# Kernel tuning notes

Measured on AMD Instinct MI355X. Metric: run time of the kernel, lower is better.

Reference implementation:

```python
import jax, jax.numpy as jnp
import numpy as np

B, N, NC = 8, 25200, 80           # YOLOv5-640 / COCO raw output
CONF_THRES = 0.25                  # init conf_threshold
IOU_THRES = 0.45                   # init iou_threshold
PATCH_CONF = 0.001                 # hard-coded patch_conf in forward
GN = jnp.array([640.0, 640.0, 640.0, 640.0], dtype=jnp.float32)  # img_size[[1,0,1,0]]
MAX_WH = 4096.0                    # class offset for class-aware NMS
K_CLEAN = 512                      # fixed-size cap on NMS candidates (clean branch)
K_PATCH = 1024                     # fixed-size cap on NMS candidates (patch branch)
MAX_DET_CLEAN = 1000
MAX_DET_PATCH = 30000
NEG = jnp.float32(-1e30)


def _xywh2xyxy(x):
    xy, wh = x[..., :2], x[..., 2:4]
    return jnp.concatenate([xy - wh * 0.5, xy + wh * 0.5], axis=-1)


def _pairwise_iou(a, b):
    # a: [A,4] xyxy, b: [B,4] xyxy -> [A,B] jaccard overlap
    tl = jnp.maximum(a[:, None, :2], b[None, :, :2])
    br = jnp.minimum(a[:, None, 2:4], b[None, :, 2:4])
    wh = jnp.clip(br - tl, 0.0)
    inter = wh[..., 0] * wh[..., 1]
    area_a = (a[:, 2] - a[:, 0]) * (a[:, 3] - a[:, 1])
    area_b = (b[:, 2] - b[:, 0]) * (b[:, 3] - b[:, 1])
    union = area_a[:, None] + area_b[None, :] - inter
    union = jnp.where(union > 0, union, 1.0)  # guard degenerate boxes
    return inter / union


def _nms_single(pred, conf_thres, K, max_det):
    # pred: [N, 5+nc]. Fixed-size (padded/masked) greedy NMS, class-aware via MAX_WH offset.
    obj = pred[:, 4]
    cls_conf = pred[:, 5:] * obj[:, None]          # x[:,5:] *= x[:,4:5]
    conf = jnp.max(cls_conf, axis=-1)
    cls = jnp.argmax(cls_conf, axis=-1)
    box = _xywh2xyxy(pred[:, :4])
    valid = (obj > conf_thres) & (conf > conf_thres)
    scores = jnp.where(valid, conf, NEG)
    top_scores, idx = jax.lax.top_k(scores, K)     # sorted desc, like torchvision NMS ordering
    boxes = box[idx]
    cls_k = cls[idx]
    valid_k = top_scores > conf_thres
    boxes_off = boxes + cls_k.astype(boxes.dtype)[:, None] * MAX_WH
    iou = jax.lax.stop_gradient(_pairwise_iou(boxes_off, boxes_off))
    ar = jnp.arange(K)

    def step(keep, i):
        sup = keep[i] & (iou[i] > IOU_THRES) & (ar > i)
        return keep & (~sup), None

    keep, _ = jax.lax.scan(step, valid_k, jnp.arange(K))
    rank = jnp.cumsum(keep.astype(jnp.int32))
    keep = keep & (rank <= max_det)
    return boxes, cls_k, keep


def _image_loss(cb, cc, ck, pb, pc, pk):
    # per clean detection: max IoU over kept patch boxes of the same class (0 if none)
    iou = _pairwise_iou(cb / GN, pb / GN)          # [K_CLEAN, K_PATCH]
    mask = ck[:, None] & pk[None, :] & (cc[:, None] == pc[None, :])
    tm = jnp.max(jnp.where(mask, iou, 0.0), axis=1)
    s = jnp.sum(jnp.where(ck, tm, 0.0))
    n = jnp.sum(ck.astype(jnp.float32))
    return s, n


def _forward(output_clean, output_patch):
    cb, cc, ck = jax.vmap(lambda p: _nms_single(p, CONF_THRES, K_CLEAN, MAX_DET_CLEAN))(output_clean)
    pb, pc, pk = jax.vmap(lambda p: _nms_single(p, PATCH_CONF, K_PATCH, MAX_DET_PATCH))(output_patch)
    s, n = jax.vmap(_image_loss)(cb, cc, ck, pb, pc, pk)
    total, cnt = jnp.sum(s), jnp.sum(n)
    return jnp.where(cnt > 0, 1.0 - total / jnp.maximum(cnt, 1.0), jnp.float32(1.0))


def _make_pred(key):
    ka, kb, kc, kd = jax.random.split(key, 4)
    cxcy = jax.random.uniform(ka, (B, N, 2), jnp.float32, 20.0, 620.0)
    wh = jax.random.uniform(kb, (B, N, 2), jnp.float32, 2.0, 150.0)
    obj = jax.random.uniform(kc, (B, N, 1), jnp.float32)
    clsp = jax.random.uniform(kd, (B, N, NC), jnp.float32)
    return jnp.concatenate([cxcy, wh, obj, clsp], axis=-1)


def setup_inputs() -> dict:
    key = jax.random.key(0)
    k1, k2 = jax.random.split(key)
    return {"output_clean": _make_pred(k1), "output_patch": _make_pred(k2)}


def reference(output_clean, output_patch):
    return _forward(output_clean, output_patch)
```

## Files before the change

kernel.cpp:

```cpp
#include <hip/hip_runtime.h>


static constexpr int NB   = 8;
static constexpr int NA   = 25200;
static constexpr int NCLS = 80;
static constexpr int CH   = 85;
static constexpr int NT   = 16;
static constexpr int KMAX = 1024;
static constexpr int NBIN = 32768;
static constexpr int PSH  = 17;
static constexpr int CAP  = 2048;
static constexpr int IOB  = 34;

static constexpr size_t OFF_KEYS = 0;
static constexpr size_t OFF_CLS  = OFF_KEYS + (size_t)NT * NA * 4;
static constexpr size_t OFF_BOX  = OFF_CLS  + (size_t)NT * NA * 4;
static constexpr size_t OFF_CLSK = OFF_BOX  + (size_t)NT * KMAX * 16;
static constexpr size_t OFF_VALK = OFF_CLSK + (size_t)NT * KMAX * 4;
static constexpr size_t OFF_KEEP = OFF_VALK + (size_t)NT * KMAX * 4;
static constexpr size_t OFF_SUP  = OFF_KEEP + (size_t)NT * 16 * 8;
static constexpr size_t OFF_DIAG = OFF_SUP  + (size_t)NT * KMAX * 16 * 8;
static constexpr size_t OFF_PART = OFF_DIAG + (size_t)NT * KMAX * 8;
static constexpr size_t OFF_CNT  = OFF_PART + 512;

__device__ __forceinline__ unsigned okey(float f) {
  unsigned u = __float_as_uint(f);
  return (u & 0x80000000u) ? ~u : (u | 0x80000000u);
}

__device__ __forceinline__ unsigned long long shflx64(unsigned long long v, int m) {
  unsigned lo = (unsigned)v, hi = (unsigned)(v >> 32);
  lo = __shfl_xor(lo, m);
  hi = __shfl_xor(hi, m);
  return ((unsigned long long)hi << 32) | lo;
}

__global__ __launch_bounds__(256) void k_score(const float* __restrict__ clean,
                                               const float* __restrict__ patch,
                                               unsigned* __restrict__ keys,
                                               int* __restrict__ clsArr,
                                               unsigned* __restrict__ cnt) {
#pragma clang fp contract(off)
  if (blockIdx.x == 0 && blockIdx.y == 0 && threadIdx.x == 0) *cnt = 0u;
  __shared__ float rows[4][32 * CH];
  const int t    = blockIdx.y;
  const int wave = threadIdx.x >> 6;
  const int lane = threadIdx.x & 63;
  const int a0   = blockIdx.x * 128 + wave * 32;
  if (a0 >= NA) return;
  const int nA = (NA - a0 < 32) ? (NA - a0) : 32;
  const float conf_th = (t < 8) ? 0.25f : 0.001f;
  const float* __restrict__ src = ((t < 8) ? clean : patch) + (size_t)(t & 7) * NA * CH;
  const float4* g4 = (const float4*)(src + (size_t)a0 * CH);
  float4* rows4 = (float4*)rows[wave];
  const int n4 = (nA * CH) >> 2;
#pragma unroll
  for (int c = 0; c < 11; ++c) {
    const int i = (c << 6) + lane;
    if (i < n4) {
      __builtin_amdgcn_global_load_lds(
          (const __attribute__((address_space(1))) void*)(g4 + i),
          (__attribute__((address_space(3))) void*)(rows4 + (c << 6)),
          16, 0, 2 );
    }
  }
  asm volatile("s_waitcnt vmcnt(0)" ::: "memory");
  __builtin_amdgcn_sched_barrier(0);

  const int ar = lane >> 1;
  const int q  = lane & 1;
  if (ar < nA) {
    const float* r = rows[wave] + ar * CH;
    const float obj = r[4];
    const int c0 = q * 40;
    float best = r[5 + c0] * obj;
    int bc = c0;
    for (int c = c0 + 1; c < c0 + 40; ++c) {
      float v = r[5 + c] * obj;
      if (v > best) { best = v; bc = c; }
    }
    float b1 = __shfl_down(best, 1); int c1 = __shfl_down(bc, 1);
    if (b1 > best || (b1 == best && c1 < bc)) { best = b1; bc = c1; }
    if (q == 0) {
      const bool valid = (obj > conf_th) && (best > conf_th);
      const float score = valid ? best : -1e30f;
      const int a = a0 + ar;
      keys[(size_t)t * NA + a]   = okey(score);
      clsArr[(size_t)t * NA + a] = bc;
    }
  }
}

__global__ __launch_bounds__(1024) void k_topsel(const unsigned* __restrict__ keys,
                                                 const int* __restrict__ clsArr,
                                                 const float* __restrict__ clean,
                                                 const float* __restrict__ patch,
                                                 float* __restrict__ boxesK,
                                                 int* __restrict__ clsK,
                                                 int* __restrict__ validK) {
#pragma clang fp contract(off)
  const int t = blockIdx.x;
  const unsigned K = (t < 8) ? 512u : 1024u;
  const float conf_th = (t < 8) ? 0.25f : 0.001f;
  __shared__ unsigned h32[NBIN / 2];
  __shared__ unsigned long long buf[CAP];
  __shared__ unsigned scnt[2];
  __shared__ unsigned wtot[16], wsuf[16];
  __shared__ int s_chunk;
  __shared__ unsigned s_acc, s_B;
  const int tid = threadIdx.x;
  const int lane = tid & 63, wv = tid >> 6;
  for (int i = tid; i < NBIN / 2; i += 1024) h32[i] = 0u;
  for (int i = tid; i < CAP; i += 1024) buf[i] = 0ull;
  if (tid < 2) scnt[tid] = 0u;
  __syncthreads();
  const unsigned INVKEY = okey(-1e30f);
  const unsigned* kv = keys + (size_t)t * NA;
  {
    const uint4* kv4 = (const uint4*)kv;
    unsigned invCnt = 0;
    for (int i = tid; i < NA / 4; i += 1024) {
      uint4 kq = kv4[i];
      unsigned kk[4] = {kq.x, kq.y, kq.z, kq.w};
#pragma unroll
      for (int c = 0; c < 4; ++c) {
        if (kk[c] == INVKEY) {
          ++invCnt;
        } else {
          unsigned b = kk[c] >> PSH;
          atomicAdd(&h32[b >> 1], 1u << ((b & 1) * 16));
        }
      }
    }
    for (int off = 32; off > 0; off >>= 1) invCnt += __shfl_down(invCnt, off);
    if (lane == 0 && invCnt) {
      unsigned b = INVKEY >> PSH;
      atomicAdd(&h32[b >> 1], invCnt << ((b & 1) * 16));
    }
  }
  __syncthreads();
  unsigned cnt_c = 0;
  for (int i = 0; i < 16; ++i) {
    unsigned v = h32[tid * 16 + i];
    cnt_c += (v & 0xFFFFu) + (v >> 16);
  }
  unsigned s = cnt_c;
  for (int off = 1; off < 64; off <<= 1) {
    unsigned v = __shfl_down(s, off);
    if (lane + off < 64) s += v;
  }
  if (lane == 0) wtot[wv] = s;
  __syncthreads();
  if (tid < 16) {
    unsigned acc = 0;
    for (int w2 = 15; w2 > tid; --w2) acc += wtot[w2];
    wsuf[tid] = acc;
  }
  __syncthreads();
  const unsigned suf = s + wsuf[wv];
  if (suf >= K && suf - cnt_c < K) { s_chunk = tid; s_acc = suf - cnt_c; }
  __syncthreads();
  if (tid == 0) {
    unsigned acc = s_acc;
    unsigned res = (unsigned)(s_chunk * 32);
    for (int i = 31; i >= 0; --i) {
      int bb = s_chunk * 32 + i;
      unsigned v = h32[bb >> 1];
      unsigned c2 = (bb & 1) ? (v >> 16) : (v & 0xFFFFu);
      if (acc + c2 >= K) { res = (unsigned)bb; break; }
      acc += c2;
    }
    s_B = res;
  }
  __syncthreads();
  const unsigned B = s_B;
  const unsigned long long lowmask =
      (lane == 0) ? 0ull : (0xFFFFFFFFFFFFFFFFull >> (64 - lane));
  for (int i = tid; i < 25600; i += 1024) {
    const bool inb = (i < NA);
    unsigned key = inb ? kv[i] : 0u;
    unsigned p = key >> PSH;
    const bool hi = inb && (p > B);
    const bool eq = inb && (p == B);
    const unsigned long long item =
        ((unsigned long long)key << 32) | (unsigned)(~(unsigned)i);
    unsigned long long mh = __ballot(hi);
    if (mh) {
      int leader = (int)__ffsll(mh) - 1;
      unsigned base2 = 0;
      if (lane == leader) base2 = atomicAdd(&scnt[0], (unsigned)__popcll(mh));
      base2 = __shfl(base2, leader);
      if (hi) {
        unsigned pos = base2 + (unsigned)__popcll(mh & lowmask);
        if (pos < 1024u) buf[pos] = item;
      }
    }
    unsigned long long me = __ballot(eq);
    if (me) {
      int leader = (int)__ffsll(me) - 1;
      unsigned base2 = 0;
      if (lane == leader) base2 = atomicAdd(&scnt[1], (unsigned)__popcll(me));
      base2 = __shfl(base2, leader);
      if (eq) {
        unsigned pos = base2 + (unsigned)__popcll(me & lowmask);
        if (pos < 1024u) buf[1024 + pos] = item;
      }
    }
  }
  __syncthreads();
  {
    const int e0 = wv * 128 + lane;
    const int e1 = e0 + 64;
    unsigned long long r0 = buf[e0], r1 = buf[e1];
    for (int kk2 = 2; kk2 <= CAP; kk2 <<= 1) {
      for (int j = kk2 >> 1; j > 0; j >>= 1) {
        if (j >= 128) {
          buf[e0] = r0; buf[e1] = r1;
          __syncthreads();
          unsigned long long o0 = buf[e0 ^ j];
          unsigned long long o1 = buf[e1 ^ j];
          const bool mx = (((e0 & kk2) == 0) == ((e0 & j) == 0));
          r0 = mx ? (r0 > o0 ? r0 : o0) : (r0 < o0 ? r0 : o0);
          r1 = mx ? (r1 > o1 ? r1 : o1) : (r1 < o1 ? r1 : o1);
          __syncthreads();
        } else if (j == 64) {
          const bool up = (e0 & kk2) == 0;
          unsigned long long mxv = r0 > r1 ? r0 : r1;
          unsigned long long mnv = r0 > r1 ? r1 : r0;
          r0 = up ? mxv : mnv;
          r1 = up ? mnv : mxv;
        } else {
          unsigned long long o0 = shflx64(r0, j);
          unsigned long long o1 = shflx64(r1, j);
          const bool up0 = (e0 & kk2) == 0;
          const bool up1 = (e1 & kk2) == 0;
          const bool lo  = (lane & j) == 0;
          const bool m0 = (up0 == lo), m1 = (up1 == lo);
          r0 = m0 ? (r0 > o0 ? r0 : o0) : (r0 < o0 ? r0 : o0);
          r1 = m1 ? (r1 > o1 ? r1 : o1) : (r1 < o1 ? r1 : o1);
        }
      }
    }
    buf[e0] = r0; buf[e1] = r1;
  }
  __syncthreads();
  const float* __restrict__ src = ((t < 8) ? clean : patch) + (size_t)(t & 7) * NA * CH;
  const unsigned vkey = okey(conf_th);
  for (int k = tid; k < (int)K; k += 1024) {
    unsigned long long v = buf[k];
    unsigned key = (unsigned)(v >> 32);
    int idx = (int)(~(unsigned)(v & 0xFFFFFFFFull));
    if (idx < 0 || idx >= NA) idx = 0;
    const float* r = src + (size_t)idx * CH;
    float cx = r[0], cy = r[1], w = r[2], h = r[3];
    float hw = w * 0.5f, hh = h * 0.5f;
    float* bo = boxesK + ((size_t)t * KMAX + k) * 4;
    bo[0] = cx - hw; bo[1] = cy - hh; bo[2] = cx + hw; bo[3] = cy + hh;
    clsK[t * KMAX + k]   = clsArr[(size_t)t * NA + idx];
    validK[t * KMAX + k] = (key > vkey) ? 1 : 0;
  }
}

__global__ __launch_bounds__(256) void k_ioumat(const float* __restrict__ boxesK,
                                                const int* __restrict__ clsK,
                                                unsigned long long* __restrict__ sup,
                                                unsigned long long* __restrict__ diag) {
#pragma clang fp contract(off)
  const int t  = blockIdx.y;
  const int K  = (t < 8) ? 512 : 1024;
  const int lw = (t < 8) ? 3 : 4;
  const int nw = 1 << lw;
  const int npair = (nw * (nw + 1)) / 2;
  const int total = npair * 64;
  if (blockIdx.x * 256 >= total) return;
  __shared__ float X1[KMAX + 16], Y1[KMAX + 16], X2[KMAX + 16], Y2[KMAX + 16], AR[KMAX + 16];
  for (int i = threadIdx.x; i < K; i += 256) {
    const float* bo = boxesK + ((size_t)t * KMAX + i) * 4;
    float off = (float)clsK[t * KMAX + i] * 4096.0f;
    float x1 = bo[0] + off, y1 = bo[1] + off, x2 = bo[2] + off, y2 = bo[3] + off;
    const int ip = i + (i >> 6);
    X1[ip] = x1; Y1[ip] = y1; X2[ip] = x2; Y2[ip] = y2;
    AR[ip] = (x2 - x1) * (y2 - y1);
  }
  __syncthreads();
  unsigned long long* supt = sup + (size_t)t * (KMAX * 16);
  for (int widx = blockIdx.x * 256 + threadIdx.x; widx < total; widx += IOB * 256) {
    int p = widx >> 6;
    int row = widx & 63;
    int rb = 0, pr = p;
    while (pr >= nw - rb) { pr -= nw - rb; ++rb; }
    const int wc = rb + pr;
    const int i = rb * 64 + row;
    const int ipi = i + rb;
    const float x1i = X1[ipi], y1i = Y1[ipi], x2i = X2[ipi], y2i = Y2[ipi], ai = AR[ipi];
    unsigned long long m = 0ull;
    const int jb = (wc << 6) + wc;
    const bool offd = (wc > rb);
#pragma unroll 4
    for (int l = 0; l < 64; ++l) {
      const int jp = jb + l;
      float tlx = fmaxf(x1i, X1[jp]);
      float tly = fmaxf(y1i, Y1[jp]);
      float brx = fminf(x2i, X2[jp]);
      float bry = fminf(y2i, Y2[jp]);
      float w = fmaxf(brx - tlx, 0.0f);
      float h = fmaxf(bry - tly, 0.0f);
      float inter = w * h;
      float uni = (ai + AR[jp]) - inter;
      uni = (uni > 0.0f) ? uni : 1.0f;
      float iou = inter / uni;
      bool hit = (iou > 0.45f) && (offd || ((wc << 6) + l > i));
      m |= hit ? (1ull << l) : 0ull;
    }
    supt[(size_t)i * nw + wc] = m;
    if (wc == rb) diag[(size_t)t * KMAX + i] = m;
  }
}

__global__ __launch_bounds__(64) void k_greedy(const unsigned long long* __restrict__ sup,
                                               const unsigned long long* __restrict__ diag,
                                               const int* __restrict__ validK,
                                               unsigned long long* __restrict__ keepw) {
  const int t  = blockIdx.x;
  const int K  = (t < 8) ? 512 : 1024;
  const int lw = (t < 8) ? 3 : 4;
  const int nw = 1 << lw;
  const int lane = threadIdx.x;
  __shared__ unsigned long long sdiag[KMAX];
  const unsigned long long* dg = diag + (size_t)t * KMAX;
  for (int i = lane; i < K; i += 64) sdiag[i] = dg[i];
  int v16[16];
#pragma unroll
  for (int W = 0; W < 16; ++W)
    v16[W] = (W < nw) ? validK[t * KMAX + W * 64 + lane] : 0;
  unsigned long long vkeep = 0ull;
#pragma unroll
  for (int W = 0; W < 16; ++W)
    if (W < nw) {
      unsigned long long bl = __ballot(v16[W] != 0);
      if (lane == W) vkeep = bl;
    }
  __syncthreads();
  const int w = lane & (nw - 1);
  const int b = lane >> lw;
  const int r0 = b * nw;
  const unsigned long long* base = sup + (size_t)t * (KMAX * 16);
  unsigned long long remv = 0ull;
  for (int W = 0; W < nw; ++W) {
    unsigned long long vv[16];
    if (W + 1 < nw) {
#pragma unroll
      for (int j = 0; j < 16; ++j)
        vv[j] = (j < nw) ? base[(size_t)(W * 64 + r0 + j) * nw + w] : 0ull;
    }
    unsigned long long cur = __shfl(vkeep, W) & ~__shfl(remv, W);
    for (int rb = 0; rb < 64; rb += 16) {
      unsigned long long tm[16];
#pragma unroll
      for (int i2 = 0; i2 < 16; ++i2) tm[i2] = sdiag[W * 64 + rb + i2];
#pragma unroll
      for (int i2 = 0; i2 < 16; ++i2) {
        unsigned long long msk = 0ull - ((cur >> (rb + i2)) & 1ull);
        cur &= ~(tm[i2] & msk);
      }
    }
    if (lane == 0) keepw[t * 16 + W] = cur;
    if (W + 1 < nw) {
      unsigned long long part = 0ull;
#pragma unroll
      for (int j = 0; j < 16; ++j) {
        bool take = (j < nw) && (w > W) && ((cur >> (r0 + j)) & 1ull);
        part |= take ? vv[j] : 0ull;
      }
      for (int s = nw; s < 64; s <<= 1) part |= __shfl_xor(part, s);
      remv |= part;
    }
  }
}

__global__ __launch_bounds__(1024) void k_loss(const float* __restrict__ boxesK,
                                               const int* __restrict__ clsK,
                                               const unsigned long long* __restrict__ keepw,
                                               float* __restrict__ part,
                                               unsigned* __restrict__ cnt,
                                               float* __restrict__ out) {
#pragma clang fp contract(off)
  const int img = blockIdx.y;
  const int chunk = blockIdx.x;
  const int tp = 8 + img;
  __shared__ float px1[KMAX], py1[KMAX], px2[KMAX], py2[KMAX], pa[KMAX];
  __shared__ int pcls[KMAX];
  __shared__ float red[1024];
  __shared__ unsigned s_last;
  for (int j = threadIdx.x; j < KMAX; j += 1024) {
    const float* bo = boxesK + ((size_t)tp * KMAX + j) * 4;
    float x1 = bo[0] / 640.0f, y1 = bo[1] / 640.0f;
    float x2 = bo[2] / 640.0f, y2 = bo[3] / 640.0f;
    px1[j] = x1; py1[j] = y1; px2[j] = x2; py2[j] = y2;
    pa[j] = (x2 - x1) * (y2 - y1);
    int kept = (int)((keepw[tp * 16 + (j >> 6)] >> (j & 63)) & 1ull);
    pcls[j] = kept ? clsK[tp * KMAX + j] : -1;
  }
  __syncthreads();
  const int row = chunk * 64 + (threadIdx.x & 63);
  const int stripe = threadIdx.x >> 6;
  const int ck = (int)((keepw[img * 16 + (row >> 6)] >> (row & 63)) & 1ull);
  const float* bo = boxesK + ((size_t)img * KMAX + row) * 4;
  float cx1 = bo[0] / 640.0f, cy1 = bo[1] / 640.0f;
  float cx2 = bo[2] / 640.0f, cy2 = bo[3] / 640.0f;
  float ca = (cx2 - cx1) * (cy2 - cy1);
  const int ccls = clsK[img * KMAX + row];
  float m = 0.0f;
  if (ck) {
    const int j0 = stripe * 64;
    for (int j = j0; j < j0 + 64; ++j) {
      if (pcls[j] == ccls) {
        float tlx = fmaxf(cx1, px1[j]);
        float tly = fmaxf(cy1, py1[j]);
        float brx = fminf(cx2, px2[j]);
        float bry = fminf(cy2, py2[j]);
        float w = fmaxf(brx - tlx, 0.0f);
        float h = fmaxf(bry - tly, 0.0f);
        float inter = w * h;
        float uni = (ca + pa[j]) - inter;
        uni = (uni > 0.0f) ? uni : 1.0f;
        m = fmaxf(m, inter / uni);
      }
    }
  }
  red[threadIdx.x] = m;
  __syncthreads();
  if (threadIdx.x < 64) {
    float mm = red[threadIdx.x];
#pragma unroll
    for (int s = 1; s < 16; ++s) mm = fmaxf(mm, red[threadIdx.x + 64 * s]);
    float sv = ck ? mm : 0.0f;
    float nv = ck ? 1.0f : 0.0f;
    for (int off = 32; off > 0; off >>= 1) {
      sv += __shfl_down(sv, off);
      nv += __shfl_down(nv, off);
    }
    if (threadIdx.x == 0) {
      int b = img * 8 + chunk;
      part[b * 2 + 0] = sv;
      part[b * 2 + 1] = nv;
      __threadfence();
      unsigned old = atomicAdd(cnt, 1u);
      s_last = (old == 63u) ? 1u : 0u;
    }
  }
  __syncthreads();
  if (s_last && threadIdx.x < 64) {
    __threadfence();
    volatile const float* vp = part;
    float sv = vp[threadIdx.x * 2 + 0];
    float nv = vp[threadIdx.x * 2 + 1];
    for (int off = 32; off > 0; off >>= 1) {
      sv += __shfl_down(sv, off);
      nv += __shfl_down(nv, off);
    }
    if (threadIdx.x == 0) out[0] = (nv > 0.0f) ? (1.0f - sv / fmaxf(nv, 1.0f)) : 1.0f;
  }
}

extern "C" void kernel_launch(void* const* d_in, const int* in_sizes, int n_in,
                              void* d_out, int out_size, void* d_ws, size_t ws_size,
                              hipStream_t stream) {
  const float* clean = (const float*)d_in[0];
  const float* patch = (const float*)d_in[1];
  char* ws = (char*)d_ws;
  unsigned* keys            = (unsigned*)(ws + OFF_KEYS);
  int* clsArr               = (int*)(ws + OFF_CLS);
  float* boxesK             = (float*)(ws + OFF_BOX);
  int* clsK                 = (int*)(ws + OFF_CLSK);
  int* validK               = (int*)(ws + OFF_VALK);
  unsigned long long* keepw = (unsigned long long*)(ws + OFF_KEEP);
  unsigned long long* sup   = (unsigned long long*)(ws + OFF_SUP);
  unsigned long long* diag  = (unsigned long long*)(ws + OFF_DIAG);
  float* part               = (float*)(ws + OFF_PART);
  unsigned* cnt             = (unsigned*)(ws + OFF_CNT);
  float* out                = (float*)d_out;

  k_score  <<<dim3((NA + 127) / 128, NT), 256, 0, stream>>>(clean, patch, keys, clsArr, cnt);
  k_topsel <<<NT, 1024, 0, stream>>>(keys, clsArr, clean, patch, boxesK, clsK, validK);
  k_ioumat <<<dim3(IOB, NT), 256, 0, stream>>>(boxesK, clsK, sup, diag);
  k_greedy <<<NT, 64, 0, stream>>>(sup, diag, validK, keepw);
  k_loss   <<<dim3(8, NB), 1024, 0, stream>>>(boxesK, clsK, keepw, part, cnt, out);
}
```

Baseline: 249.9 us.

## Double-buffer greedy NMS suppression blocks into LDS with async global loads

The greedy NMS kernel is templated on the word count, so the 512 and 1024 candidate cases get fully unrolled code. Each next 64-row suppression block is prefetched into a double-buffered LDS area with global_load_lds while the current block's diagonal resolution runs, with explicit vmcnt waits. The goal is to hide global-load latency on the serial single-wave critical path. It relies on hand-counted vmcnt values and removes the __syncthreads, which is safe only because the block is a single wave.

New measurement: 255.0 us. 1.02x slower.

```diff
diff --git a/kernel.cpp b/kernel.cpp
--- a/kernel.cpp
+++ b/kernel.cpp
@@ -317,65 +317,104 @@
   }
 }
 
+template <int LW>
+__device__ __forceinline__ void greedy_body(const unsigned long long* __restrict__ sup,
+                                            const unsigned long long* __restrict__ diag,
+                                            const int* __restrict__ validK,
+                                            unsigned long long* __restrict__ keepw,
+                                            int t, unsigned long long* sdiag,
+                                            unsigned long long* bufLDS) {
+  constexpr int NW = 1 << LW;
+  constexpr int K  = NW * 64;
+  constexpr int CHUNKS = NW / 2;
+  constexpr int BLKU64 = 64 * NW;
+  const int lane = threadIdx.x;
+  const unsigned long long* base = sup + (size_t)t * (KMAX * 16);
+  {
+    const char* blk0 = (const char*)base;
+#pragma unroll
+    for (int c = 0; c < CHUNKS; ++c) {
+      __builtin_amdgcn_global_load_lds(
+          (const __attribute__((address_space(1))) void*)(blk0 + (size_t)(c * 64 + lane) * 16),
+          (__attribute__((address_space(3))) void*)((char*)bufLDS + c * 1024),
+          16, 0, 0);
+    }
+  }
+  const unsigned long long* dg = diag + (size_t)t * KMAX;
+  for (int i = lane; i < K; i += 64) sdiag[i] = dg[i];
+  int v16[NW];
+#pragma unroll
+  for (int W = 0; W < NW; ++W) v16[W] = validK[t * KMAX + W * 64 + lane];
+  unsigned long long vkeep = 0ull;
+#pragma unroll
+  for (int W = 0; W < NW; ++W) {
+    unsigned long long bl = __ballot(v16[W] != 0);
+    if (lane == W) vkeep = bl;
+  }
+  asm volatile("s_waitcnt vmcnt(0)" ::: "memory");
+  __builtin_amdgcn_sched_barrier(0);
+
+  const int w  = lane & (NW - 1);
+  const int b  = lane >> LW;
+  const int r0 = b * NW;
+  unsigned long long remv = 0ull;
+  unsigned long long curs[NW];
+#pragma unroll
+  for (int W = 0; W < NW; ++W) {
+    if (W + 1 < NW) {
+      const char* blkn = (const char*)(base + (size_t)(W + 1) * BLKU64);
+      char* dst = (char*)(bufLDS + ((W + 1) & 1) * BLKU64);
+#pragma unroll
+      for (int c = 0; c < CHUNKS; ++c) {
+        __builtin_amdgcn_global_load_lds(
+            (const __attribute__((address_space(1))) void*)(blkn + (size_t)(c * 64 + lane) * 16),
+            (__attribute__((address_space(3))) void*)(dst + c * 1024),
+            16, 0, 0);
+      }
+    }
+    unsigned long long cur = __shfl(vkeep, W) & ~__shfl(remv, W);
+    for (int rb = 0; rb < 64; rb += 16) {
+      unsigned long long tm[16];
+#pragma unroll
+      for (int i2 = 0; i2 < 16; ++i2) tm[i2] = sdiag[W * 64 + rb + i2];
+#pragma unroll
+      for (int i2 = 0; i2 < 16; ++i2) {
+        unsigned long long msk = 0ull - ((cur >> (rb + i2)) & 1ull);
+        cur &= ~(tm[i2] & msk);
+      }
+    }
+    curs[W] = cur;
+    if (W + 1 < NW) {
+      if constexpr (NW == 16) { asm volatile("s_waitcnt vmcnt(8)" ::: "memory"); }
+      else                    { asm volatile("s_waitcnt vmcnt(4)" ::: "memory"); }
+      __builtin_amdgcn_sched_barrier(0);
+      const unsigned long long* bw = bufLDS + (W & 1) * BLKU64;
+      unsigned long long part = 0ull;
+#pragma unroll
+      for (int j = 0; j < NW; ++j) {
+        unsigned long long v = bw[(r0 + j) * NW + w];
+        bool take = (w > W) && ((cur >> (r0 + j)) & 1ull);
+        part |= take ? v : 0ull;
+      }
+      for (int s = NW; s < 64; s <<= 1) part |= __shfl_xor(part, s);
+      remv |= part;
+    }
+  }
+  if (lane == 0) {
+#pragma unroll
+    for (int W = 0; W < NW; ++W) keepw[t * 16 + W] = curs[W];
+  }
+}
+
 __global__ __launch_bounds__(64) void k_greedy(const unsigned long long* __restrict__ sup,
                                                const unsigned long long* __restrict__ diag,
                                                const int* __restrict__ validK,
                                                unsigned long long* __restrict__ keepw) {
-  const int t  = blockIdx.x;
-  const int K  = (t < 8) ? 512 : 1024;
-  const int lw = (t < 8) ? 3 : 4;
-  const int nw = 1 << lw;
-  const int lane = threadIdx.x;
   __shared__ unsigned long long sdiag[KMAX];
-  const unsigned long long* dg = diag + (size_t)t * KMAX;
-  for (int i = lane; i < K; i += 64) sdiag[i] = dg[i];
-  int v16[16];
-#pragma unroll
-  for (int W = 0; W < 16; ++W)
-    v16[W] = (W < nw) ? validK[t * KMAX + W * 64 + lane] : 0;
-  unsigned long long vkeep = 0ull;
-#pragma unroll
-  for (int W = 0; W < 16; ++W)
-    if (W < nw) {
-      unsigned long long bl = __ballot(v16[W] != 0);
-      if (lane == W) vkeep = bl;
-    }
-  __syncthreads();
-  const int w = lane & (nw - 1);
-  const int b = lane >> lw;
-  const int r0 = b * nw;
-  const unsigned long long* base = sup + (size_t)t * (KMAX * 16);
-  unsigned long long remv = 0ull;
-  for (int W = 0; W < nw; ++W) {
-    unsigned long long vv[16];
-    if (W + 1 < nw) {
-#pragma unroll
-      for (int j = 0; j < 16; ++j)
-        vv[j] = (j < nw) ? base[(size_t)(W * 64 + r0 + j) * nw + w] : 0ull;
-    }
-    unsigned long long cur = __shfl(vkeep, W) & ~__shfl(remv, W);
-    for (int rb = 0; rb < 64; rb += 16) {
-      unsigned long long tm[16];
-#pragma unroll
-      for (int i2 = 0; i2 < 16; ++i2) tm[i2] = sdiag[W * 64 + rb + i2];
-#pragma unroll
-      for (int i2 = 0; i2 < 16; ++i2) {
-        unsigned long long msk = 0ull - ((cur >> (rb + i2)) & 1ull);
-        cur &= ~(tm[i2] & msk);
-      }
-    }
-    if (lane == 0) keepw[t * 16 + W] = cur;
-    if (W + 1 < nw) {
-      unsigned long long part = 0ull;
-#pragma unroll
-      for (int j = 0; j < 16; ++j) {
-        bool take = (j < nw) && (w > W) && ((cur >> (r0 + j)) & 1ull);
-        part |= take ? vv[j] : 0ull;
-      }
-      for (int s = nw; s < 64; s <<= 1) part |= __shfl_xor(part, s);
-      remv |= part;
-    }
-  }
+  __shared__ unsigned long long buf2[2 * 64 * 16];
+  const int t = blockIdx.x;
+  if (t < 8) greedy_body<3>(sup, diag, validK, keepw, t, sdiag, buf2);
+  else       greedy_body<4>(sup, diag, validK, keepw, t, sdiag, buf2);
 }
 
 __global__ __launch_bounds__(1024) void k_loss(const float* __restrict__ boxesK,
```

## Fuse IoU-matrix and greedy NMS kernels with per-image completion counters

Applied to the files above, without the earlier changes.

Merges the IoU bitmask kernel and the greedy NMS kernel into one launch. The extra trailing blocks spin on a per-image atomic counter until all IoU blocks for that image finish, then run the greedy pass. This removes one kernel launch and its boundary gap, so images whose matrices finish early can start their greedy pass sooner. The spin-wait relies on the IoU blocks being scheduled before or alongside the waiting blocks, and adds atomics and fences.

Measured after the change: 293.6 us. 17.5% more time.

```diff
diff --git a/kernel.cpp b/kernel.cpp
--- a/kernel.cpp
+++ b/kernel.cpp
@@ -22,6 +22,7 @@
 static constexpr size_t OFF_DIAG = OFF_SUP  + (size_t)NT * KMAX * 16 * 8;
 static constexpr size_t OFF_PART = OFF_DIAG + (size_t)NT * KMAX * 8;
 static constexpr size_t OFF_CNT  = OFF_PART + 512;
+static constexpr size_t OFF_DONE = OFF_CNT + 16;
 
 __device__ __forceinline__ unsigned okey(float f) {
   unsigned u = __float_as_uint(f);
@@ -39,9 +40,13 @@
                                                const float* __restrict__ patch,
                                                unsigned* __restrict__ keys,
                                                int* __restrict__ clsArr,
-                                               unsigned* __restrict__ cnt) {
+                                               unsigned* __restrict__ cnt,
+                                               unsigned* __restrict__ done) {
 #pragma clang fp contract(off)
-  if (blockIdx.x == 0 && blockIdx.y == 0 && threadIdx.x == 0) *cnt = 0u;
+  if (blockIdx.x == 0 && blockIdx.y == 0) {
+    if (threadIdx.x == 0) *cnt = 0u;
+    if (threadIdx.x < 16) done[threadIdx.x] = 0u;
+  }
   __shared__ float rows[4][32 * CH];
   const int t    = blockIdx.y;
   const int wave = threadIdx.x >> 6;
@@ -261,72 +266,88 @@
   }
 }
 
-__global__ __launch_bounds__(256) void k_ioumat(const float* __restrict__ boxesK,
-                                                const int* __restrict__ clsK,
-                                                unsigned long long* __restrict__ sup,
-                                                unsigned long long* __restrict__ diag) {
+__global__ __launch_bounds__(256) void k_iougr(const float* __restrict__ boxesK,
+                                               const int* __restrict__ clsK,
+                                               const int* __restrict__ validK,
+                                               unsigned long long* __restrict__ sup,
+                                               unsigned long long* __restrict__ diag,
+                                               unsigned long long* __restrict__ keepw,
+                                               unsigned* __restrict__ done) {
 #pragma clang fp contract(off)
-  const int t  = blockIdx.y;
+  __shared__ __align__(16) float smem[5 * (KMAX + 16)];
+  const int bid = blockIdx.x;
+  if (bid < IOB * NT) {
+    const int t  = bid / IOB;
+    const int bx = bid % IOB;
+    const int K  = (t < 8) ? 512 : 1024;
+    const int lw = (t < 8) ? 3 : 4;
+    const int nw = 1 << lw;
+    const int npair = (nw * (nw + 1)) / 2;
+    const int total = npair * 64;
+    if (bx * 256 < total) {
+      float* X1 = smem;
+      float* Y1 = X1 + (KMAX + 16);
+      float* X2 = Y1 + (KMAX + 16);
+      float* Y2 = X2 + (KMAX + 16);
+      float* AR = Y2 + (KMAX + 16);
+      for (int i = threadIdx.x; i < K; i += 256) {
+        const float* bo = boxesK + ((size_t)t * KMAX + i) * 4;
+        float off = (float)clsK[t * KMAX + i] * 4096.0f;
+        float x1 = bo[0] + off, y1 = bo[1] + off, x2 = bo[2] + off, y2 = bo[3] + off;
+        const int ip = i + (i >> 6);
+        X1[ip] = x1; Y1[ip] = y1; X2[ip] = x2; Y2[ip] = y2;
+        AR[ip] = (x2 - x1) * (y2 - y1);
+      }
+      __syncthreads();
+      unsigned long long* supt = sup + (size_t)t * (KMAX * 16);
+      for (int widx = bx * 256 + threadIdx.x; widx < total; widx += IOB * 256) {
+        int p = widx >> 6;
+        int row = widx & 63;
+        int rb = 0, pr = p;
+        while (pr >= nw - rb) { pr -= nw - rb; ++rb; }
+        const int wc = rb + pr;
+        const int i = rb * 64 + row;
+        const int ipi = i + rb;
+        const float x1i = X1[ipi], y1i = Y1[ipi], x2i = X2[ipi], y2i = Y2[ipi], ai = AR[ipi];
+        unsigned long long m = 0ull;
+        const int jb = (wc << 6) + wc;
+        const bool offd = (wc > rb);
+#pragma unroll 4
+        for (int l = 0; l < 64; ++l) {
+          const int jp = jb + l;
+          float tlx = fmaxf(x1i, X1[jp]);
+          float tly = fmaxf(y1i, Y1[jp]);
+          float brx = fminf(x2i, X2[jp]);
+          float bry = fminf(y2i, Y2[jp]);
+          float w = fmaxf(brx - tlx, 0.0f);
+          float h = fmaxf(bry - tly, 0.0f);
+          float inter = w * h;
+          float uni = (ai + AR[jp]) - inter;
+          uni = (uni > 0.0f) ? uni : 1.0f;
+          float iou = inter / uni;
+          bool hit = (iou > 0.45f) && (offd || ((wc << 6) + l > i));
+          m |= hit ? (1ull << l) : 0ull;
+        }
+        supt[(size_t)i * nw + wc] = m;
+        if (wc == rb) diag[(size_t)t * KMAX + i] = m;
+      }
+    }
+    __threadfence();
+    __syncthreads();
+    if (threadIdx.x == 0) atomicAdd(&done[t], 1u);
+    return;
+  }
+  if (threadIdx.x >= 64) return;
+  const int t = bid - IOB * NT;
+  const int lane = threadIdx.x;
+  if (lane == 0) {
+    while (atomicAdd(&done[t], 0u) < (unsigned)IOB) __builtin_amdgcn_s_sleep(2);
+  }
+  __threadfence();
   const int K  = (t < 8) ? 512 : 1024;
   const int lw = (t < 8) ? 3 : 4;
   const int nw = 1 << lw;
-  const int npair = (nw * (nw + 1)) / 2;
-  const int total = npair * 64;
-  if (blockIdx.x * 256 >= total) return;
-  __shared__ float X1[KMAX + 16], Y1[KMAX + 16], X2[KMAX + 16], Y2[KMAX + 16], AR[KMAX + 16];
-  for (int i = threadIdx.x; i < K; i += 256) {
-    const float* bo = boxesK + ((size_t)t * KMAX + i) * 4;
-    float off = (float)clsK[t * KMAX + i] * 4096.0f;
-    float x1 = bo[0] + off, y1 = bo[1] + off, x2 = bo[2] + off, y2 = bo[3] + off;
-    const int ip = i + (i >> 6);
-    X1[ip] = x1; Y1[ip] = y1; X2[ip] = x2; Y2[ip] = y2;
-    AR[ip] = (x2 - x1) * (y2 - y1);
-  }
-  __syncthreads();
-  unsigned long long* supt = sup + (size_t)t * (KMAX * 16);
-  for (int widx = blockIdx.x * 256 + threadIdx.x; widx < total; widx += IOB * 256) {
-    int p = widx >> 6;
-    int row = widx & 63;
-    int rb = 0, pr = p;
-    while (pr >= nw - rb) { pr -= nw - rb; ++rb; }
-    const int wc = rb + pr;
-    const int i = rb * 64 + row;
-    const int ipi = i + rb;
-    const float x1i = X1[ipi], y1i = Y1[ipi], x2i = X2[ipi], y2i = Y2[ipi], ai = AR[ipi];
-    unsigned long long m = 0ull;
-    const int jb = (wc << 6) + wc;
-    const bool offd = (wc > rb);
-#pragma unroll 4
-    for (int l = 0; l < 64; ++l) {
-      const int jp = jb + l;
-      float tlx = fmaxf(x1i, X1[jp]);
-      float tly = fmaxf(y1i, Y1[jp]);
-      float brx = fminf(x2i, X2[jp]);
-      float bry = fminf(y2i, Y2[jp]);
-      float w = fmaxf(brx - tlx, 0.0f);
-      float h = fmaxf(bry - tly, 0.0f);
-      float inter = w * h;
-      float uni = (ai + AR[jp]) - inter;
-      uni = (uni > 0.0f) ? uni : 1.0f;
-      float iou = inter / uni;
-      bool hit = (iou > 0.45f) && (offd || ((wc << 6) + l > i));
-      m |= hit ? (1ull << l) : 0ull;
-    }
-    supt[(size_t)i * nw + wc] = m;
-    if (wc == rb) diag[(size_t)t * KMAX + i] = m;
-  }
-}
-
-__global__ __launch_bounds__(64) void k_greedy(const unsigned long long* __restrict__ sup,
-                                               const unsigned long long* __restrict__ diag,
-                                               const int* __restrict__ validK,
-                                               unsigned long long* __restrict__ keepw) {
-  const int t  = blockIdx.x;
-  const int K  = (t < 8) ? 512 : 1024;
-  const int lw = (t < 8) ? 3 : 4;
-  const int nw = 1 << lw;
-  const int lane = threadIdx.x;
-  __shared__ unsigned long long sdiag[KMAX];
+  unsigned long long* sdiag = (unsigned long long*)smem;
   const unsigned long long* dg = diag + (size_t)t * KMAX;
   for (int i = lane; i < K; i += 64) sdiag[i] = dg[i];
   int v16[16];
@@ -479,11 +500,11 @@
   unsigned long long* diag  = (unsigned long long*)(ws + OFF_DIAG);
   float* part               = (float*)(ws + OFF_PART);
   unsigned* cnt             = (unsigned*)(ws + OFF_CNT);
+  unsigned* done            = (unsigned*)(ws + OFF_DONE);
   float* out                = (float*)d_out;
 
-  k_score  <<<dim3((NA + 127) / 128, NT), 256, 0, stream>>>(clean, patch, keys, clsArr, cnt);
+  k_score  <<<dim3((NA + 127) / 128, NT), 256, 0, stream>>>(clean, patch, keys, clsArr, cnt, done);
   k_topsel <<<NT, 1024, 0, stream>>>(keys, clsArr, clean, patch, boxesK, clsK, validK);
-  k_ioumat <<<dim3(IOB, NT), 256, 0, stream>>>(boxesK, clsK, sup, diag);
-  k_greedy <<<NT, 64, 0, stream>>>(sup, diag, validK, keepw);
+  k_iougr  <<<IOB * NT + NT, 256, 0, stream>>>(boxesK, clsK, validK, sup, diag, keepw, done);
   k_loss   <<<dim3(8, NB), 1024, 0, stream>>>(boxesK, clsK, keepw, part, cnt, out);
 }
```
